# Performance work log

Hardware: AMD Instinct MI355X
Metric: run time of the kernel (lower is better)

## Reference

```python
import jax, jax.numpy as jnp
import numpy as np

ALPHA, GAMMA = 0.25, 2.0
COST_CLASS, COST_BBOX, COST_GIOU = 2.0, 5.0, 2.0
EPS = 1e-8


def box_cxcywh_to_xyxy(b):
    cx, cy, w, h = b[..., 0], b[..., 1], b[..., 2], b[..., 3]
    return jnp.stack([cx - 0.5 * w, cy - 0.5 * h, cx + 0.5 * w, cy + 0.5 * h], axis=-1)


def generalized_box_iou(boxes1, boxes2):
    # boxes1: [N,4] xyxy, boxes2: [M,4] xyxy -> [N,M] GIoU
    area1 = (boxes1[:, 2] - boxes1[:, 0]) * (boxes1[:, 3] - boxes1[:, 1])
    area2 = (boxes2[:, 2] - boxes2[:, 0]) * (boxes2[:, 3] - boxes2[:, 1])
    lt = jnp.maximum(boxes1[:, None, :2], boxes2[None, :, :2])   # [N,M,2]
    rb = jnp.minimum(boxes1[:, None, 2:], boxes2[None, :, 2:])   # [N,M,2]
    wh = jnp.clip(rb - lt, 0.0)
    inter = wh[..., 0] * wh[..., 1]
    union = area1[:, None] + area2[None, :] - inter
    iou = inter / union
    # smallest enclosing box
    lt_c = jnp.minimum(boxes1[:, None, :2], boxes2[None, :, :2])
    rb_c = jnp.maximum(boxes1[:, None, 2:], boxes2[None, :, 2:])
    wh_c = jnp.clip(rb_c - lt_c, 0.0)
    area_c = wh_c[..., 0] * wh_c[..., 1]
    return iou - (area_c - union) / area_c


def setup_inputs() -> dict:
    key = jax.random.key(0)
    k1, k2, k3, k4 = jax.random.split(key, 4)
    BS, NQ, NC, NT = 16, 900, 91, 960
    pred_logits = jax.random.normal(k1, (BS, NQ, NC), dtype=jnp.float32)
    pred_boxes = jax.random.uniform(k2, (BS, NQ, 4), dtype=jnp.float32)
    tgt_ids = jax.random.randint(k3, (NT,), 0, NC, dtype=jnp.int64)
    tgt_bbox = jax.random.uniform(k4, (NT, 4), dtype=jnp.float32)
    return {"pred_logits": pred_logits, "pred_boxes": pred_boxes,
            "tgt_ids": tgt_ids, "tgt_bbox": tgt_bbox}


def reference(pred_logits, pred_boxes, tgt_ids, tgt_bbox):
    bs, nq, _ = pred_logits.shape
    out_prob = jax.nn.sigmoid(pred_logits.reshape(bs * nq, -1))      # [BN, C]
    out_bbox = pred_boxes.reshape(bs * nq, 4)                         # [BN, 4]
    # focal-style classification cost, gathered at target class ids
    neg_cost = (1.0 - ALPHA) * out_prob ** GAMMA * (-jnp.log(1.0 - out_prob + EPS))
    pos_cost = ALPHA * (1.0 - out_prob) ** GAMMA * (-jnp.log(out_prob + EPS))
    cost_class = pos_cost[:, tgt_ids] - neg_cost[:, tgt_ids]          # [BN, NT]
    # pairwise L1 distance between boxes (cxcywh space), like torch.cdist(p=1)
    cost_bbox = jnp.sum(jnp.abs(out_bbox[:, None, :] - tgt_bbox[None, :, :]), axis=-1)
    cost_giou = -generalized_box_iou(box_cxcywh_to_xyxy(out_bbox),
                                     box_cxcywh_to_xyxy(tgt_bbox))    # [BN, NT]
    C = COST_BBOX * cost_bbox + COST_CLASS * cost_class + COST_GIOU * cost_giou
    return C.reshape(bs, nq, -1)
```

## Files before the change

### kernel.cpp

```cpp
#include <hip/hip_runtime.h>
#include <math.h>


#define ALPHA_F   0.25f
#define COST_CLS  2.0f
#define COST_BBOX 5.0f
#define COST_GIOU 2.0f
#define EPS_F     1e-8f

constexpr int THREADS = 256;

__device__ __forceinline__ float focal_entry(float x) {
    const float p  = 1.0f / (1.0f + __expf(-x));
    const float om = 1.0f - p;
    const float neg = (1.0f - ALPHA_F) * p * p * (-__logf(om + EPS_F));
    const float pos = ALPHA_F * om * om        * (-__logf(p  + EPS_F));
    return COST_CLS * (pos - neg) + COST_GIOU;
}

template<int NC, int NT>
__global__ __launch_bounds__(THREADS) void matcher_kernel_s(
    const float* __restrict__ logits,
    const float* __restrict__ boxes,
    const int*   __restrict__ tids,
    const float* __restrict__ tboxes,
    float*       __restrict__ out)
{
    constexpr int ROWS = 2;
    constexpr int JPT  = 4;
    constexpr int NJT  = NT / JPT;
    constexpr int NTAB = ROWS * NC;
    constexpr int CSTR = 3;

    __shared__ float s_cls[NC * CSTR];

    const int tid  = threadIdx.x;
    const int row0 = blockIdx.x * ROWS;
    const bool active = tid < NJT;

    float x = 0.0f;
    if (tid < NTAB)
        x = logits[(size_t)row0 * NC + tid];

    float4 tb[JPT];
    int ic[JPT] = {0, 0, 0, 0};
    if (active) {
        #pragma unroll
        for (int k = 0; k < JPT; ++k) {
            tb[k] = reinterpret_cast<const float4*>(tboxes)[tid + k * NJT];
            ic[k] = tids[tid + k * NJT];
        }
    } else {
        #pragma unroll
        for (int k = 0; k < JPT; ++k) tb[k] = make_float4(0.f, 0.f, 0.f, 0.f);
    }

    if (tid < NTAB) {
        const int r = (tid >= NC) ? 1 : 0;
        const int c = tid - (r ? NC : 0);
        s_cls[c * CSTR + r] = focal_entry(x);
    }
    __syncthreads();

    if (!active) return;

    float cc0[JPT], cc1[JPT];
    #pragma unroll
    for (int k = 0; k < JPT; ++k) {
        const float* cp = s_cls + ic[k] * CSTR;
        cc0[k] = cp[0];
        cc1[k] = cp[1];
    }

    float* __restrict__ obase = out + (size_t)row0 * NT + tid;
    #pragma unroll
    for (int r = 0; r < ROWS; ++r) {
        const float4 pb = reinterpret_cast<const float4*>(boxes)[row0 + r];
        const float px0 = pb.x - 0.5f * pb.z, py0 = pb.y - 0.5f * pb.w;
        const float px1 = pb.x + 0.5f * pb.z, py1 = pb.y + 0.5f * pb.w;
        const float parea = pb.z * pb.w;

        #pragma unroll
        for (int k = 0; k < JPT; ++k) {
            const float4 t = tb[k];
            const float hw = 0.5f * t.z, hh = 0.5f * t.w;
            const float tx0 = t.x - hw, tx1 = t.x + hw;
            const float ty0 = t.y - hh, ty1 = t.y + hh;
            const float tarea = t.z * t.w;
            const float l1 = (fabsf(pb.x - t.x) + fabsf(pb.y - t.y))
                           + (fabsf(pb.z - t.z) + fabsf(pb.w - t.w));
            const float iwr = fminf(px1, tx1) - fmaxf(px0, tx0);
            const float ihr = fminf(py1, ty1) - fmaxf(py0, ty0);
            const float inter = fmaxf(iwr, 0.0f) * fmaxf(ihr, 0.0f);
            const float uni = (parea + tarea) - inter;
            const float cw = (pb.z + t.z) - iwr;
            const float ch = (pb.w + t.w) - ihr;
            const float carea = cw * ch;
            const float num  = fmaf(inter, carea, uni * uni);
            const float rcpd = __builtin_amdgcn_rcpf(uni * carea);
            const float ctab = (r == 0) ? cc0[k] : cc1[k];
            const float base = fmaf(COST_BBOX, l1, ctab);
            const float v = fmaf(-2.0f * num, rcpd, base);
            __builtin_nontemporal_store(v, obase + (size_t)r * NT + k * NJT);
        }
    }
}

constexpr int GROWS = 8;
__global__ __launch_bounds__(THREADS) void matcher_kernel_g(
    const float* __restrict__ logits, const float* __restrict__ boxes,
    const int* __restrict__ tids, const float* __restrict__ tboxes,
    float* __restrict__ out, int BN, int NC, int NT)
{
    extern __shared__ float s_cls_g[];
    const int tid  = threadIdx.x;
    const int row0 = blockIdx.x * GROWS;
    const int nrows = (BN - row0 < GROWS) ? (BN - row0) : GROWS;

    for (int t = tid; t < nrows * NC; t += THREADS) {
        const int r = t / NC, c = t - r * NC;
        const float x = logits[(size_t)(row0 + r) * NC + c];
        const float p  = 1.0f / (1.0f + expf(-x));
        const float om = 1.0f - p;
        const float neg = (1.0f - ALPHA_F) * p * p * (-logf(om + EPS_F));
        const float pos = ALPHA_F * om * om        * (-logf(p + EPS_F));
        s_cls_g[r * NC + c] = pos - neg;
    }
    __syncthreads();

    for (int r = 0; r < nrows; ++r) {
        const int row = row0 + r;
        const float4 pb = reinterpret_cast<const float4*>(boxes)[row];
        const float px0 = pb.x - 0.5f * pb.z, py0 = pb.y - 0.5f * pb.w;
        const float px1 = pb.x + 0.5f * pb.z, py1 = pb.y + 0.5f * pb.w;
        const float parea = pb.z * pb.w;
        for (int j = tid; j < NT; j += THREADS) {
            const float4 b = reinterpret_cast<const float4*>(tboxes)[j];
            const float bx0 = b.x - 0.5f * b.z, by0 = b.y - 0.5f * b.w;
            const float bx1 = b.x + 0.5f * b.z, by1 = b.y + 0.5f * b.w;
            const float l1 = fabsf(pb.x - b.x) + fabsf(pb.y - b.y)
                           + fabsf(pb.z - b.z) + fabsf(pb.w - b.w);
            const float iw = fmaxf(fminf(px1, bx1) - fmaxf(px0, bx0), 0.0f);
            const float ih = fmaxf(fminf(py1, by1) - fmaxf(py0, by0), 0.0f);
            const float inter = iw * ih;
            const float uni = parea + b.z * b.w - inter;
            const float iou = inter / uni;
            const float cw = fmaxf(px1, bx1) - fminf(px0, bx0);
            const float ch = fmaxf(py1, by1) - fminf(py0, by0);
            const float carea = cw * ch;
            const float giou = iou - (carea - uni) / carea;
            const float ccls = s_cls_g[r * NC + tids[j]];
            out[(size_t)row * NT + j] = COST_BBOX * l1 + COST_CLS * ccls - COST_GIOU * giou;
        }
        __syncthreads();
    }
}

extern "C" void kernel_launch(void* const* d_in, const int* in_sizes, int n_in,
                              void* d_out, int out_size, void* d_ws, size_t ws_size,
                              hipStream_t stream) {
    const float* logits = (const float*)d_in[0];
    const float* boxes  = (const float*)d_in[1];
    const int*   tids   = (const int*)d_in[2];
    const float* tboxes = (const float*)d_in[3];
    float* out = (float*)d_out;

    const int BN = in_sizes[1] / 4;
    const int NC = in_sizes[0] / BN;
    const int NT = in_sizes[2];

    if (NC == 91 && NT == 960 && BN % 2 == 0) {
        matcher_kernel_s<91, 960><<<BN / 2, THREADS, 0, stream>>>(
            logits, boxes, tids, tboxes, out);
    } else {
        const int grid = (BN + GROWS - 1) / GROWS;
        const size_t shmem = (size_t)GROWS * NC * sizeof(float);
        matcher_kernel_g<<<grid, THREADS, shmem, stream>>>(
            logits, boxes, tids, tboxes, out, BN, NC, NT);
    }
}
```

Baseline: 20.82 us.

## Process four rows per block, overlapping second class table build with output

Each block now handles four prediction rows instead of two, using two shared class-cost tables. The second table's focal computation is done after the first barrier, so it overlaps with writing the first two output rows, and a second barrier guards the later rows. The aim is to amortize the per-block target box and id loads and hide the transcendental cost of the focal entries. In exchange the grid is halved to 3600 blocks, which lowers parallelism, and an extra barrier is added.

After: 20.92 us. Within noise of the previous version (+0.5%).

```diff
diff --git a/kernel.cpp b/kernel.cpp
--- a/kernel.cpp
+++ b/kernel.cpp
@@ -19,28 +19,30 @@
 }
 
 template<int NC, int NT>
-__global__ __launch_bounds__(THREADS) void matcher_kernel_s(
+__global__ __launch_bounds__(THREADS) void matcher_kernel_p(
     const float* __restrict__ logits,
     const float* __restrict__ boxes,
     const int*   __restrict__ tids,
     const float* __restrict__ tboxes,
     float*       __restrict__ out)
 {
-    constexpr int ROWS = 2;
     constexpr int JPT  = 4;
     constexpr int NJT  = NT / JPT;
-    constexpr int NTAB = ROWS * NC;
+    constexpr int NTAB = 2 * NC;
     constexpr int CSTR = 3;
 
-    __shared__ float s_cls[NC * CSTR];
+    __shared__ float s_cls[2][NC * CSTR];
 
     const int tid  = threadIdx.x;
-    const int row0 = blockIdx.x * ROWS;
+    const int row0 = blockIdx.x * 4;
     const bool active = tid < NJT;
-
-    float x = 0.0f;
-    if (tid < NTAB)
-        x = logits[(size_t)row0 * NC + tid];
+    const bool tabth  = tid < NTAB;
+
+    float x0 = 0.0f, x1 = 0.0f;
+    if (tabth) {
+        x0 = logits[(size_t)row0 * NC + tid];
+        x1 = logits[(size_t)(row0 + 2) * NC + tid];
+    }
 
     float4 tb[JPT];
     int ic[JPT] = {0, 0, 0, 0};
@@ -55,53 +57,81 @@
         for (int k = 0; k < JPT; ++k) tb[k] = make_float4(0.f, 0.f, 0.f, 0.f);
     }
 
-    if (tid < NTAB) {
-        const int r = (tid >= NC) ? 1 : 0;
-        const int c = tid - (r ? NC : 0);
-        s_cls[c * CSTR + r] = focal_entry(x);
+    int tr = 0, tc = 0;
+    if (tabth) {
+        tr = (tid >= NC) ? 1 : 0;
+        tc = tid - (tr ? NC : 0);
+        s_cls[0][tc * CSTR + tr] = focal_entry(x0);
     }
     __syncthreads();
 
-    if (!active) return;
-
-    float cc0[JPT], cc1[JPT];
-    #pragma unroll
-    for (int k = 0; k < JPT; ++k) {
-        const float* cp = s_cls + ic[k] * CSTR;
-        cc0[k] = cp[0];
-        cc1[k] = cp[1];
-    }
-
-    float* __restrict__ obase = out + (size_t)row0 * NT + tid;
-    #pragma unroll
-    for (int r = 0; r < ROWS; ++r) {
-        const float4 pb = reinterpret_cast<const float4*>(boxes)[row0 + r];
-        const float px0 = pb.x - 0.5f * pb.z, py0 = pb.y - 0.5f * pb.w;
-        const float px1 = pb.x + 0.5f * pb.z, py1 = pb.y + 0.5f * pb.w;
-        const float parea = pb.z * pb.w;
-
-        #pragma unroll
-        for (int k = 0; k < JPT; ++k) {
-            const float4 t = tb[k];
-            const float hw = 0.5f * t.z, hh = 0.5f * t.w;
-            const float tx0 = t.x - hw, tx1 = t.x + hw;
-            const float ty0 = t.y - hh, ty1 = t.y + hh;
-            const float tarea = t.z * t.w;
-            const float l1 = (fabsf(pb.x - t.x) + fabsf(pb.y - t.y))
-                           + (fabsf(pb.z - t.z) + fabsf(pb.w - t.w));
-            const float iwr = fminf(px1, tx1) - fmaxf(px0, tx0);
-            const float ihr = fminf(py1, ty1) - fmaxf(py0, ty0);
-            const float inter = fmaxf(iwr, 0.0f) * fmaxf(ihr, 0.0f);
-            const float uni = (parea + tarea) - inter;
-            const float cw = (pb.z + t.z) - iwr;
-            const float ch = (pb.w + t.w) - ihr;
-            const float carea = cw * ch;
-            const float num  = fmaf(inter, carea, uni * uni);
-            const float rcpd = __builtin_amdgcn_rcpf(uni * carea);
-            const float ctab = (r == 0) ? cc0[k] : cc1[k];
-            const float base = fmaf(COST_BBOX, l1, ctab);
-            const float v = fmaf(-2.0f * num, rcpd, base);
-            __builtin_nontemporal_store(v, obase + (size_t)r * NT + k * NJT);
+    if (tabth)
+        s_cls[1][tc * CSTR + tr] = focal_entry(x1);
+
+    if (active) {
+        float* __restrict__ obase = out + (size_t)row0 * NT + tid;
+        #pragma unroll
+        for (int r = 0; r < 2; ++r) {
+            const float4 pb = reinterpret_cast<const float4*>(boxes)[row0 + r];
+            const float px0 = pb.x - 0.5f * pb.z, py0 = pb.y - 0.5f * pb.w;
+            const float px1 = pb.x + 0.5f * pb.z, py1 = pb.y + 0.5f * pb.w;
+            const float parea = pb.z * pb.w;
+            #pragma unroll
+            for (int k = 0; k < JPT; ++k) {
+                const float ctab = s_cls[0][ic[k] * CSTR + r];
+                const float4 t = tb[k];
+                const float tarea = t.z * t.w;
+                const float l1 = (fabsf(pb.x - t.x) + fabsf(pb.y - t.y))
+                               + (fabsf(pb.z - t.z) + fabsf(pb.w - t.w));
+                const float tx0 = t.x - 0.5f * t.z, tx1 = t.x + 0.5f * t.z;
+                const float ty0 = t.y - 0.5f * t.w, ty1 = t.y + 0.5f * t.w;
+                const float iwr = fminf(px1, tx1) - fmaxf(px0, tx0);
+                const float ihr = fminf(py1, ty1) - fmaxf(py0, ty0);
+                const float inter = fmaxf(iwr, 0.0f) * fmaxf(ihr, 0.0f);
+                const float uni = (parea + tarea) - inter;
+                const float cw = (pb.z + t.z) - iwr;
+                const float ch = (pb.w + t.w) - ihr;
+                const float carea = cw * ch;
+                const float num  = fmaf(inter, carea, uni * uni);
+                const float rcpd = __builtin_amdgcn_rcpf(uni * carea);
+                const float base = fmaf(COST_BBOX, l1, ctab);
+                const float v = fmaf(-2.0f * num, rcpd, base);
+                __builtin_nontemporal_store(v, obase + (size_t)r * NT + k * NJT);
+            }
+        }
+    }
+    __syncthreads();
+
+    if (active) {
+        float* __restrict__ obase = out + (size_t)(row0 + 2) * NT + tid;
+        #pragma unroll
+        for (int r = 0; r < 2; ++r) {
+            const float4 pb = reinterpret_cast<const float4*>(boxes)[row0 + 2 + r];
+            const float px0 = pb.x - 0.5f * pb.z, py0 = pb.y - 0.5f * pb.w;
+            const float px1 = pb.x + 0.5f * pb.z, py1 = pb.y + 0.5f * pb.w;
+            const float parea = pb.z * pb.w;
+            #pragma unroll
+            for (int k = 0; k < JPT; ++k) {
+                const float ctab = s_cls[1][ic[k] * CSTR + r];
+                const float4 t = tb[k];
+                const float tarea = t.z * t.w;
+                const float l1 = (fabsf(pb.x - t.x) + fabsf(pb.y - t.y))
+                               + (fabsf(pb.z - t.z) + fabsf(pb.w - t.w));
+                const float tx0 = t.x - 0.5f * t.z, tx1 = t.x + 0.5f * t.z;
+                const float ty0 = t.y - 0.5f * t.w, ty1 = t.y + 0.5f * t.w;
+                const float iwr = fminf(px1, tx1) - fmaxf(px0, tx0);
+                const float ihr = fminf(py1, ty1) - fmaxf(py0, ty0);
+                const float inter = fmaxf(iwr, 0.0f) * fmaxf(ihr, 0.0f);
+                const float uni = (parea + tarea) - inter;
+                const float cw = (pb.z + t.z) - iwr;
+                const float ch = (pb.w + t.w) - ihr;
+                const float carea = cw * ch;
+                const float num  = fmaf(inter, carea, uni * uni);
+                const float rcpd = __builtin_amdgcn_rcpf(uni * carea);
+                const float base = fmaf(COST_BBOX, l1, ctab);
+                const float v = fmaf(-2.0f * num, rcpd, base);
+                __builtin_nontemporal_store(v, obase + (size_t)r * NT + k * NJT);
+            }
         }
     }
 }
@@ -136,10 +166,10 @@
         const float parea = pb.z * pb.w;
         for (int j = tid; j < NT; j += THREADS) {
             const float4 b = reinterpret_cast<const float4*>(tboxes)[j];
+            const float l1 = fabsf(pb.x - b.x) + fabsf(pb.y - b.y)
+                           + fabsf(pb.z - b.z) + fabsf(pb.w - b.w);
             const float bx0 = b.x - 0.5f * b.z, by0 = b.y - 0.5f * b.w;
             const float bx1 = b.x + 0.5f * b.z, by1 = b.y + 0.5f * b.w;
-            const float l1 = fabsf(pb.x - b.x) + fabsf(pb.y - b.y)
-                           + fabsf(pb.z - b.z) + fabsf(pb.w - b.w);
             const float iw = fmaxf(fminf(px1, bx1) - fmaxf(px0, bx0), 0.0f);
             const float ih = fmaxf(fminf(py1, by1) - fmaxf(py0, by0), 0.0f);
             const float inter = iw * ih;
@@ -169,8 +199,8 @@
     const int NC = in_sizes[0] / BN;
     const int NT = in_sizes[2];
 
-    if (NC == 91 && NT == 960 && BN % 2 == 0) {
-        matcher_kernel_s<91, 960><<<BN / 2, THREADS, 0, stream>>>(
+    if (NC == 91 && NT == 960 && BN % 4 == 0) {
+        matcher_kernel_p<91, 960><<<BN / 4, THREADS, 0, stream>>>(
             logits, boxes, tids, tboxes, out);
     } else {
         const int grid = (BN + GROWS - 1) / GROWS;
```
